# Kernel optimization log

Hardware: AMD Instinct MI355X
Metric: run time of the kernel (lower is better)

The kernel has to match this reference:

```python
import jax, jax.numpy as jnp
import numpy as np

B, T, D, H = 1024, 128, 300, 100
FORGET_BIAS = 1.0


def _lstm_final_c(x, W, b):
    """Run a BasicLSTMCell over x:[B,T,D]; return final cell state c:[B,H].
    Gate order (TF BasicLSTMCell): i, j, f, o from [x,h] @ W + b, W:[D+H,4H].
    """
    Bv = x.shape[0]
    c0 = jnp.zeros((Bv, H), x.dtype)
    h0 = jnp.zeros((Bv, H), x.dtype)

    def step(carry, xt):
        c, h = carry
        z = jnp.concatenate([xt, h], axis=-1) @ W + b  # [B,4H]
        i, j, f, o = jnp.split(z, 4, axis=-1)
        c2 = c * jax.nn.sigmoid(f + FORGET_BIAS) + jax.nn.sigmoid(i) * jnp.tanh(j)
        h2 = jnp.tanh(c2) * jax.nn.sigmoid(o)
        return (c2, h2), None

    (cT, _), _ = jax.lax.scan(step, (c0, h0), jnp.swapaxes(x, 0, 1))  # scan over time
    return cT


def _bi_rnn_c(x, W_fw, b_fw, W_bw, b_bw):
    # full sequence_length => backward cell consumes time-reversed input
    c_fw = _lstm_final_c(x, W_fw, b_fw)
    c_bw = _lstm_final_c(x[:, ::-1, :], W_bw, b_bw)
    return jnp.concatenate([c_fw, c_bw], axis=1)  # [B,2H]


def setup_inputs() -> dict:
    key = jax.random.key(0)
    ks = jax.random.split(key, 6)
    s = 0.05
    return {
        "premises": jax.random.normal(ks[0], (B, T, D), jnp.float32),
        "hypotheses": jax.random.normal(ks[1], (B, T, D), jnp.float32),
        "Wp_fw": jax.random.normal(ks[2], (D + H, 4 * H), jnp.float32) * s,
        "bp_fw": jnp.zeros((4 * H,), jnp.float32),
        "Wp_bw": jax.random.normal(ks[3], (D + H, 4 * H), jnp.float32) * s,
        "bp_bw": jnp.zeros((4 * H,), jnp.float32),
        "Wh_fw": jax.random.normal(ks[4], (D + H, 4 * H), jnp.float32) * s,
        "bh_fw": jnp.zeros((4 * H,), jnp.float32),
        "Wh_bw": jax.random.normal(ks[5], (D + H, 4 * H), jnp.float32) * s,
        "bh_bw": jnp.zeros((4 * H,), jnp.float32),
    }


def reference(premises, hypotheses, Wp_fw, bp_fw, Wp_bw, bp_bw,
              Wh_fw, bh_fw, Wh_bw, bh_bw):
    premise_out = _bi_rnn_c(premises, Wp_fw, bp_fw, Wp_bw, bp_bw)      # [B,2H]
    hypothesis_out = _bi_rnn_c(hypotheses, Wh_fw, bh_fw, Wh_bw, bh_bw)  # [B,2H]
    return jnp.concatenate([premise_out, hypothesis_out], axis=1)      # [B,4H]
```

## Files before the change

kernel.cpp:

```cpp
#include <hip/hip_runtime.h>
#include <hip/hip_bf16.h>

#define T_STEPS 128
#define D_IN    300
#define H_DIM   100
#define KDIM    400
#define KSTRIDE 424
#define WAVES   8
#define BLOCK   (WAVES * 64)
#define MROWS   16
#define NRES    3
#define LN2E    1.44269504f
#define LN2E2   2.88539008f

typedef __attribute__((ext_vector_type(8))) short bf16x8;
typedef __attribute__((ext_vector_type(4))) float f32x4;

__device__ __forceinline__ ushort f2bf(float f) {
    uint u = __float_as_uint(f);
    u += 0x7FFFu + ((u >> 16) & 1u);
    return (ushort)(u >> 16);
}
__device__ __forceinline__ uint cvt_pk_bf16(float lo, float hi) {
    uint r;
    asm("v_cvt_pk_bf16_f32 %0, %1, %2" : "=v"(r) : "v"(lo), "v"(hi));
    return r;
}
__device__ __forceinline__ bf16x8 gload16(const ushort* p) {
    bf16x8 r;
    asm volatile("global_load_dwordx4 %0, %1, off" : "=v"(r) : "v"(p));
    return r;
}

__device__ __forceinline__ float lstm_gate(const f32x4 z, float& c) {
    float ei = __builtin_amdgcn_exp2f(-z[0]);
    float ej = __builtin_amdgcn_exp2f(fminf(-z[1], 126.0f));
    float ef = __builtin_amdgcn_exp2f(-z[2]);
    float eo = __builtin_amdgcn_exp2f(-z[3]);
    float rf  = __builtin_amdgcn_rcpf(1.0f + ef);
    float rij = __builtin_amdgcn_rcpf((1.0f + ei) * (1.0f + ej));
    float c2 = c * rf + (1.0f - ej) * rij;
    c = c2;
    float ec = __builtin_amdgcn_exp2f(fminf(-LN2E2 * c2, 126.0f));
    return (1.0f - ec) * __builtin_amdgcn_rcpf((1.0f + ec) * (1.0f + eo));
}

__global__ __launch_bounds__(256) void prep_w(
    const float* __restrict__ W0, const float* __restrict__ W1,
    const float* __restrict__ W2, const float* __restrict__ W3,
    ushort* __restrict__ Wt)
{
    int idx = blockIdx.x * 256 + threadIdx.x;
    const int total = 4 * 400 * KSTRIDE;
    if (idx >= total) return;
    int c   = idx / (400 * KSTRIDE);
    int rem = idx - c * (400 * KSTRIDE);
    int p   = rem / KSTRIDE;
    int k   = rem - p * KSTRIDE;
    const float* W = (c == 0) ? W0 : (c == 1) ? W1 : (c == 2) ? W2 : W3;
    const int g = p & 3;
    const float scale = (g == 1) ? LN2E2 : LN2E;
    float v = 0.0f;
    if (k < KDIM) v = W[k * 400 + g * 100 + (p >> 2)] * scale;
    Wt[idx] = f2bf(v);
}

__global__ __launch_bounds__(BLOCK, 2) void lstm_mfma(
    const float* __restrict__ premises,
    const float* __restrict__ hypotheses,
    const float* __restrict__ b0, const float* __restrict__ b1,
    const float* __restrict__ b2, const float* __restrict__ b3,
    const ushort* __restrict__ Wt,
    float* __restrict__ out)
{
    __shared__ ushort xh[2][MROWS * KSTRIDE];
    __shared__ ushort b24[13 * 512];

    const int tid = threadIdx.x;
    const int l   = tid & 63;
    const int w   = tid >> 6;
    const int combo = blockIdx.y;
    const int row0  = blockIdx.x * MROWS;
    const bool backward = (combo & 1) != 0;
    const float* x    = (combo < 2) ? premises : hypotheses;
    const float* bias = (combo == 0) ? b0 : (combo == 1) ? b1 : (combo == 2) ? b2 : b3;
    const ushort* Wc  = Wt + (size_t)combo * 400 * KSTRIDE;

    const int bn = l & 15;
    const int ul = l >> 4;

    bf16x8 bfr[NRES][13];
    #pragma unroll
    for (int i = 0; i < NRES; ++i) {
        const ushort* bp = Wc + (size_t)((3 * w + i) * 16 + bn) * KSTRIDE + ul * 8;
        #pragma unroll
        for (int ks = 0; ks < 13; ++ks)
            bfr[i][ks] = gload16(bp + ks * 32);
    }
    asm volatile("s_waitcnt vmcnt(0)" ::: "memory");

    const bool hasS = (w == WAVES - 1);
    if (w == 0) {
        const ushort* bp = Wc + (size_t)(24 * 16 + bn) * KSTRIDE + ul * 8;
        #pragma unroll
        for (int ks = 0; ks < 13; ++ks)
            *reinterpret_cast<bf16x8*>(&b24[ks * 512 + l * 8]) =
                *reinterpret_cast<const bf16x8*>(bp + ks * 32);
    }

    float bv[NRES][4], bvS[4] = {0.f, 0.f, 0.f, 0.f};
    #pragma unroll
    for (int i = 0; i < NRES; ++i) {
        int u = (3 * w + i) * 4 + ul;
        bv[i][0] = LN2E * bias[u];
        bv[i][1] = LN2E2 * bias[100 + u];
        bv[i][2] = LN2E * (bias[200 + u] + 1.0f);
        bv[i][3] = LN2E * bias[300 + u];
    }
    if (hasS) {
        int u = 96 + ul;
        bvS[0] = LN2E * bias[u];
        bvS[1] = LN2E2 * bias[100 + u];
        bvS[2] = LN2E * (bias[200 + u] + 1.0f);
        bvS[3] = LN2E * bias[300 + u];
    }

    for (int i = tid; i < 2 * MROWS * (KSTRIDE - KDIM); i += BLOCK) {
        int b = i / (MROWS * (KSTRIDE - KDIM));
        int j = i - b * (MROWS * (KSTRIDE - KDIM));
        int r = j / (KSTRIDE - KDIM);
        int k = KDIM + (j - r * (KSTRIDE - KDIM));
        xh[b][r * KSTRIDE + k] = 0;
    }
    for (int i = tid; i < MROWS * H_DIM; i += BLOCK) {
        int r = i / H_DIM;
        xh[0][r * KSTRIDE + D_IN + (i - r * H_DIM)] = 0;
    }
    {
        int t0 = backward ? (T_STEPS - 1) : 0;
        for (int c = tid; c < 1200; c += BLOCK) {
            int r = c / 75, cc = c - (c / 75) * 75;
            float4 v = *reinterpret_cast<const float4*>(
                x + ((size_t)(row0 + r) * T_STEPS + t0) * D_IN + cc * 4);
            uint2 q;
            q.x = cvt_pk_bf16(v.x, v.y);
            q.y = cvt_pk_bf16(v.z, v.w);
            *reinterpret_cast<uint2*>(&xh[0][r * KSTRIDE + cc * 4]) = q;
        }
    }
    __syncthreads();

    const uint a_off = (uint)(l & 15) * KSTRIDE + (uint)(l >> 4) * 8;
    const int  row   = l & 15;
    const bool stager = (tid < 448);
    const int sc0 = tid, sc1 = tid + 448, sc2 = tid + 896;
    const int sr0 = sc0 / 75, sd0 = sc0 - sr0 * 75;
    const int sr1 = sc1 / 75, sd1 = sc1 - sr1 * 75;
    const int sr2 = sc2 / 75, sd2 = sc2 - sr2 * 75;
    const bool has2 = (sc2 < 1200);

    float creg0 = 0.f, creg1 = 0.f, creg2 = 0.f, cregS = 0.f;

    float4 A0, A1, A2, B0, B1, B2;

    if (stager) {
        int tn = backward ? (T_STEPS - 2) : 1;
        A0 = *reinterpret_cast<const float4*>(
            x + ((size_t)(row0 + sr0) * T_STEPS + tn) * D_IN + sd0 * 4);
        A1 = *reinterpret_cast<const float4*>(
            x + ((size_t)(row0 + sr1) * T_STEPS + tn) * D_IN + sd1 * 4);
        if (has2)
            A2 = *reinterpret_cast<const float4*>(
                x + ((size_t)(row0 + sr2) * T_STEPS + tn) * D_IN + sd2 * 4);
    }

    auto step = [&](int t, float4& i0, float4& i1, float4& i2,
                           float4& u0, float4& u1, float4& u2) {
        const ushort* cur = &xh[t & 1][0];
        ushort* nxt = &xh[(t & 1) ^ 1][0];

        if (t < T_STEPS - 2 && stager) {
            int tn = backward ? (T_STEPS - 3 - t) : (t + 2);
            i0 = *reinterpret_cast<const float4*>(
                x + ((size_t)(row0 + sr0) * T_STEPS + tn) * D_IN + sd0 * 4);
            i1 = *reinterpret_cast<const float4*>(
                x + ((size_t)(row0 + sr1) * T_STEPS + tn) * D_IN + sd1 * 4);
            if (has2)
                i2 = *reinterpret_cast<const float4*>(
                    x + ((size_t)(row0 + sr2) * T_STEPS + tn) * D_IN + sd2 * 4);
        }

        f32x4 acc0 = {bv[0][0], bv[0][1], bv[0][2], bv[0][3]};
        f32x4 acc1 = {bv[1][0], bv[1][1], bv[1][2], bv[1][3]};
        f32x4 acc2 = {bv[2][0], bv[2][1], bv[2][2], bv[2][3]};
        f32x4 accS = {bvS[0], bvS[1], bvS[2], bvS[3]};
        #pragma unroll
        for (int ks = 0; ks < 13; ++ks) {
            const bf16x8 a = *reinterpret_cast<const bf16x8*>(cur + a_off + ks * 32);
            acc0 = __builtin_amdgcn_mfma_f32_16x16x32_bf16(bfr[0][ks], a, acc0, 0, 0, 0);
            acc1 = __builtin_amdgcn_mfma_f32_16x16x32_bf16(bfr[1][ks], a, acc1, 0, 0, 0);
            acc2 = __builtin_amdgcn_mfma_f32_16x16x32_bf16(bfr[2][ks], a, acc2, 0, 0, 0);
            if (hasS) {
                const bf16x8 bs = *reinterpret_cast<const bf16x8*>(&b24[ks * 512 + l * 8]);
                accS = __builtin_amdgcn_mfma_f32_16x16x32_bf16(bs, a, accS, 0, 0, 0);
            }
        }

        float h0 = lstm_gate(acc0, creg0);
        float h1 = lstm_gate(acc1, creg1);
        float h2 = lstm_gate(acc2, creg2);
        uint pk01 = cvt_pk_bf16(h0, h1);
        uint pk2  = cvt_pk_bf16(h2, h2);
        ushort* hdst = nxt + row * KSTRIDE + D_IN + (3 * w) * 4 + ul;
        hdst[0] = (ushort)(pk01 & 0xFFFFu);
        hdst[4] = (ushort)(pk01 >> 16);
        hdst[8] = (ushort)(pk2 & 0xFFFFu);
        if (hasS) {
            float hS = lstm_gate(accS, cregS);
            nxt[row * KSTRIDE + D_IN + 96 + ul] = (ushort)(cvt_pk_bf16(hS, hS) & 0xFFFFu);
        }

        if (t < T_STEPS - 1 && stager) {
            uint2 q;
            q.x = cvt_pk_bf16(u0.x, u0.y);
            q.y = cvt_pk_bf16(u0.z, u0.w);
            *reinterpret_cast<uint2*>(&nxt[sr0 * KSTRIDE + sd0 * 4]) = q;
            q.x = cvt_pk_bf16(u1.x, u1.y);
            q.y = cvt_pk_bf16(u1.z, u1.w);
            *reinterpret_cast<uint2*>(&nxt[sr1 * KSTRIDE + sd1 * 4]) = q;
            if (has2) {
                q.x = cvt_pk_bf16(u2.x, u2.y);
                q.y = cvt_pk_bf16(u2.z, u2.w);
                *reinterpret_cast<uint2*>(&nxt[sr2 * KSTRIDE + sd2 * 4]) = q;
            }
        }
        __syncthreads();
    };

    for (int t = 0; t < T_STEPS; t += 2) {
        step(t,     B0, B1, B2, A0, A1, A2);
        step(t + 1, A0, A1, A2, B0, B1, B2);
    }

    out[(size_t)(row0 + row) * 400 + combo * 100 + (3 * w) * 4 + ul]     = creg0;
    out[(size_t)(row0 + row) * 400 + combo * 100 + (3 * w + 1) * 4 + ul] = creg1;
    out[(size_t)(row0 + row) * 400 + combo * 100 + (3 * w + 2) * 4 + ul] = creg2;
    if (hasS)
        out[(size_t)(row0 + row) * 400 + combo * 100 + 96 + ul] = cregS;
}

extern "C" void kernel_launch(void* const* d_in, const int* in_sizes, int n_in,
                              void* d_out, int out_size, void* d_ws, size_t ws_size,
                              hipStream_t stream) {
    const float* premises   = (const float*)d_in[0];
    const float* hypotheses = (const float*)d_in[1];
    const float* Wp_fw = (const float*)d_in[2];
    const float* bp_fw = (const float*)d_in[3];
    const float* Wp_bw = (const float*)d_in[4];
    const float* bp_bw = (const float*)d_in[5];
    const float* Wh_fw = (const float*)d_in[6];
    const float* bh_fw = (const float*)d_in[7];
    const float* Wh_bw = (const float*)d_in[8];
    const float* bh_bw = (const float*)d_in[9];
    float* out = (float*)d_out;
    ushort* Wt = (ushort*)d_ws;

    {
        const int total = 4 * 400 * KSTRIDE;
        prep_w<<<(total + 255) / 256, 256, 0, stream>>>(Wp_fw, Wp_bw, Wh_fw, Wh_bw, Wt);
    }
    dim3 grid(1024 / MROWS, 4);
    lstm_mfma<<<grid, dim3(BLOCK), 0, stream>>>(
        premises, hypotheses,
        bp_fw, bp_bw, bh_fw, bh_bw,
        Wt, out);
}
```

Baseline: 223.6 us.

## Split LSTM GEMM into x-projection and recurrent parts, precompute next step's input term

Splits the per-step K=400 MFMA into an input part (first 288 x features) and a recurrent part (h plus the remaining 12 x features). The input part for step t+1 is computed after the gates of step t, off the serial h dependency chain. A triple-buffered x tile and a double-buffered h tile in shared memory support this. The block shrinks from 8 to 4 waves, each owning 6 gate tiles, which raises register pressure and halves occupancy.

```diff
diff --git a/kernel.cpp b/kernel.cpp
--- a/kernel.cpp
+++ b/kernel.cpp
@@ -5,11 +5,15 @@
 #define D_IN    300
 #define H_DIM   100
 #define KDIM    400
-#define KSTRIDE 424
-#define WAVES   8
-#define BLOCK   (WAVES * 64)
+#define WK      416
+#define XK      288
 #define MROWS   16
-#define NRES    3
+#define XROW    296
+#define XSLOT   (MROWS * XROW)
+#define HROW    136
+#define HSLOT   (MROWS * HROW)
+#define BLOCK   256
+#define NRES    6
 #define LN2E    1.44269504f
 #define LN2E2   2.88539008f
 
@@ -24,11 +28,6 @@
 __device__ __forceinline__ uint cvt_pk_bf16(float lo, float hi) {
     uint r;
     asm("v_cvt_pk_bf16_f32 %0, %1, %2" : "=v"(r) : "v"(lo), "v"(hi));
-    return r;
-}
-__device__ __forceinline__ bf16x8 gload16(const ushort* p) {
-    bf16x8 r;
-    asm volatile("global_load_dwordx4 %0, %1, off" : "=v"(r) : "v"(p));
     return r;
 }
 
@@ -51,12 +50,12 @@
     ushort* __restrict__ Wt)
 {
     int idx = blockIdx.x * 256 + threadIdx.x;
-    const int total = 4 * 400 * KSTRIDE;
+    const int total = 4 * 400 * WK;
     if (idx >= total) return;
-    int c   = idx / (400 * KSTRIDE);
-    int rem = idx - c * (400 * KSTRIDE);
-    int p   = rem / KSTRIDE;
-    int k   = rem - p * KSTRIDE;
+    int c   = idx / (400 * WK);
+    int rem = idx - c * (400 * WK);
+    int p   = rem / WK;
+    int k   = rem - p * WK;
     const float* W = (c == 0) ? W0 : (c == 1) ? W1 : (c == 2) ? W2 : W3;
     const int g = p & 3;
     const float scale = (g == 1) ? LN2E2 : LN2E;
@@ -65,7 +64,7 @@
     Wt[idx] = f2bf(v);
 }
 
-__global__ __launch_bounds__(BLOCK, 2) void lstm_mfma(
+__global__ __launch_bounds__(BLOCK, 1) void lstm_mfma(
     const float* __restrict__ premises,
     const float* __restrict__ hypotheses,
     const float* __restrict__ b0, const float* __restrict__ b1,
@@ -73,7 +72,8 @@
     const ushort* __restrict__ Wt,
     float* __restrict__ out)
 {
-    __shared__ ushort xh[2][MROWS * KSTRIDE];
+    __shared__ ushort xmain[3 * XSLOT];
+    __shared__ ushort hbuf[2 * HSLOT];
     __shared__ ushort b24[13 * 512];
 
     const int tid = threadIdx.x;
@@ -84,7 +84,7 @@
     const bool backward = (combo & 1) != 0;
     const float* x    = (combo < 2) ? premises : hypotheses;
     const float* bias = (combo == 0) ? b0 : (combo == 1) ? b1 : (combo == 2) ? b2 : b3;
-    const ushort* Wc  = Wt + (size_t)combo * 400 * KSTRIDE;
+    const ushort* Wc  = Wt + (size_t)combo * 400 * WK;
 
     const int bn = l & 15;
     const int ul = l >> 4;
@@ -92,16 +92,14 @@
     bf16x8 bfr[NRES][13];
     #pragma unroll
     for (int i = 0; i < NRES; ++i) {
-        const ushort* bp = Wc + (size_t)((3 * w + i) * 16 + bn) * KSTRIDE + ul * 8;
+        const ushort* bp = Wc + (size_t)((NRES * w + i) * 16 + bn) * WK + ul * 8;
         #pragma unroll
         for (int ks = 0; ks < 13; ++ks)
-            bfr[i][ks] = gload16(bp + ks * 32);
-    }
-    asm volatile("s_waitcnt vmcnt(0)" ::: "memory");
-
-    const bool hasS = (w == WAVES - 1);
+            bfr[i][ks] = *reinterpret_cast<const bf16x8*>(bp + ks * 32);
+    }
+    const bool hasS = (w == 3);
     if (w == 0) {
-        const ushort* bp = Wc + (size_t)(24 * 16 + bn) * KSTRIDE + ul * 8;
+        const ushort* bp = Wc + (size_t)(24 * 16 + bn) * WK + ul * 8;
         #pragma unroll
         for (int ks = 0; ks < 13; ++ks)
             *reinterpret_cast<bf16x8*>(&b24[ks * 512 + l * 8]) =
@@ -111,7 +109,7 @@
     float bv[NRES][4], bvS[4] = {0.f, 0.f, 0.f, 0.f};
     #pragma unroll
     for (int i = 0; i < NRES; ++i) {
-        int u = (3 * w + i) * 4 + ul;
+        int u = (NRES * w + i) * 4 + ul;
         bv[i][0] = LN2E * bias[u];
         bv[i][1] = LN2E2 * bias[100 + u];
         bv[i][2] = LN2E * (bias[200 + u] + 1.0f);
@@ -125,126 +123,169 @@
         bvS[3] = LN2E * bias[300 + u];
     }
 
-    for (int i = tid; i < 2 * MROWS * (KSTRIDE - KDIM); i += BLOCK) {
-        int b = i / (MROWS * (KSTRIDE - KDIM));
-        int j = i - b * (MROWS * (KSTRIDE - KDIM));
-        int r = j / (KSTRIDE - KDIM);
-        int k = KDIM + (j - r * (KSTRIDE - KDIM));
-        xh[b][r * KSTRIDE + k] = 0;
-    }
-    for (int i = tid; i < MROWS * H_DIM; i += BLOCK) {
-        int r = i / H_DIM;
-        xh[0][r * KSTRIDE + D_IN + (i - r * H_DIM)] = 0;
-    }
-    {
-        int t0 = backward ? (T_STEPS - 1) : 0;
-        for (int c = tid; c < 1200; c += BLOCK) {
-            int r = c / 75, cc = c - (c / 75) * 75;
+    int MR[5], MD[5];
+    bool MV[5];
+    #pragma unroll
+    for (int j = 0; j < 5; ++j) {
+        int c = tid + j * 256;
+        MV[j] = (c < 1152);
+        MR[j] = c / 72;
+        MD[j] = c - MR[j] * 72;
+    }
+    const bool tv = (tid < 48);
+    const int TR = tid / 3, TD = tid - TR * 3;
+
+    float4 T1, T2;
+
+    for (int s = 0; s < 2; ++s) {
+        int tt = backward ? (T_STEPS - 1 - s) : s;
+        #pragma unroll
+        for (int j = 0; j < 5; ++j)
+            if (MV[j]) {
+                float4 v = *reinterpret_cast<const float4*>(
+                    x + ((size_t)(row0 + MR[j]) * T_STEPS + tt) * D_IN + MD[j] * 4);
+                uint2 q;
+                q.x = cvt_pk_bf16(v.x, v.y);
+                q.y = cvt_pk_bf16(v.z, v.w);
+                *reinterpret_cast<uint2*>(&xmain[s * XSLOT + MR[j] * XROW + MD[j] * 4]) = q;
+            }
+        if (tv) {
             float4 v = *reinterpret_cast<const float4*>(
-                x + ((size_t)(row0 + r) * T_STEPS + t0) * D_IN + cc * 4);
+                x + ((size_t)(row0 + TR) * T_STEPS + tt) * D_IN + XK + TD * 4);
+            if (s == 0) {
+                uint2 q;
+                q.x = cvt_pk_bf16(v.x, v.y);
+                q.y = cvt_pk_bf16(v.z, v.w);
+                *reinterpret_cast<uint2*>(&hbuf[TR * HROW + TD * 4]) = q;
+            } else {
+                T1 = v;
+            }
+        }
+    }
+    for (int i = tid; i < MROWS * 124; i += BLOCK) {
+        int r = i / 124;
+        hbuf[r * HROW + 12 + (i - r * 124)] = 0;
+    }
+    for (int i = tid; i < MROWS * 24; i += BLOCK) {
+        int r = i / 24;
+        hbuf[HSLOT + r * HROW + 112 + (i - r * 24)] = 0;
+    }
+    __syncthreads();
+
+    const uint xoff = (uint)(l & 15) * XROW + (uint)ul * 8;
+    const uint hoff = (uint)(l & 15) * HROW + (uint)ul * 8;
+    const int  row  = l & 15;
+
+    f32x4 accA[NRES], accB[NRES], accAS, accBS;
+    #pragma unroll
+    for (int i = 0; i < NRES; ++i)
+        accA[i] = (f32x4){bv[i][0], bv[i][1], bv[i][2], bv[i][3]};
+    accAS = (f32x4){bvS[0], bvS[1], bvS[2], bvS[3]};
+    #pragma unroll
+    for (int ks = 0; ks < 9; ++ks) {
+        const bf16x8 a = *reinterpret_cast<const bf16x8*>(xmain + xoff + ks * 32);
+        #pragma unroll
+        for (int i = 0; i < NRES; ++i)
+            accA[i] = __builtin_amdgcn_mfma_f32_16x16x32_bf16(bfr[i][ks], a, accA[i], 0, 0, 0);
+        if (hasS) {
+            const bf16x8 bs = *reinterpret_cast<const bf16x8*>(&b24[ks * 512 + l * 8]);
+            accAS = __builtin_amdgcn_mfma_f32_16x16x32_bf16(bs, a, accAS, 0, 0, 0);
+        }
+    }
+
+    float creg[NRES];
+    #pragma unroll
+    for (int i = 0; i < NRES; ++i) creg[i] = 0.f;
+    float cregS = 0.f;
+
+    auto body = [&](int t, f32x4 (&accC)[NRES], f32x4& accCS,
+                           f32x4 (&accN)[NRES], f32x4& accNS,
+                           float4& Tw, float4& Ti) {
+        float4 M[5];
+        if (t <= T_STEPS - 3) {
+            int tn = backward ? (T_STEPS - 3 - t) : (t + 2);
+            #pragma unroll
+            for (int j = 0; j < 5; ++j)
+                if (MV[j])
+                    M[j] = *reinterpret_cast<const float4*>(
+                        x + ((size_t)(row0 + MR[j]) * T_STEPS + tn) * D_IN + MD[j] * 4);
+            if (tv)
+                Ti = *reinterpret_cast<const float4*>(
+                    x + ((size_t)(row0 + TR) * T_STEPS + tn) * D_IN + XK + TD * 4);
+        }
+
+        const ushort* hb = hbuf + (t & 1) * HSLOT;
+        #pragma unroll
+        for (int ks = 0; ks < 4; ++ks) {
+            const bf16x8 a = *reinterpret_cast<const bf16x8*>(hb + hoff + ks * 32);
+            #pragma unroll
+            for (int i = 0; i < NRES; ++i)
+                accC[i] = __builtin_amdgcn_mfma_f32_16x16x32_bf16(bfr[i][9 + ks], a, accC[i], 0, 0, 0);
+            if (hasS) {
+                const bf16x8 bs = *reinterpret_cast<const bf16x8*>(&b24[(9 + ks) * 512 + l * 8]);
+                accCS = __builtin_amdgcn_mfma_f32_16x16x32_bf16(bs, a, accCS, 0, 0, 0);
+            }
+        }
+
+        ushort* hw = hbuf + ((t + 1) & 1) * HSLOT;
+        #pragma unroll
+        for (int i = 0; i < NRES; ++i) {
+            float h = lstm_gate(accC[i], creg[i]);
+            hw[row * HROW + 12 + (NRES * w + i) * 4 + ul] =
+                (ushort)(cvt_pk_bf16(h, h) & 0xFFFFu);
+        }
+        if (hasS) {
+            float hS = lstm_gate(accCS, cregS);
+            hw[row * HROW + 12 + 96 + ul] = (ushort)(cvt_pk_bf16(hS, hS) & 0xFFFFu);
+        }
+        if (tv && t <= T_STEPS - 2) {
             uint2 q;
-            q.x = cvt_pk_bf16(v.x, v.y);
-            q.y = cvt_pk_bf16(v.z, v.w);
-            *reinterpret_cast<uint2*>(&xh[0][r * KSTRIDE + cc * 4]) = q;
-        }
-    }
-    __syncthreads();
-
-    const uint a_off = (uint)(l & 15) * KSTRIDE + (uint)(l >> 4) * 8;
-    const int  row   = l & 15;
-    const bool stager = (tid < 448);
-    const int sc0 = tid, sc1 = tid + 448, sc2 = tid + 896;
-    const int sr0 = sc0 / 75, sd0 = sc0 - sr0 * 75;
-    const int sr1 = sc1 / 75, sd1 = sc1 - sr1 * 75;
-    const int sr2 = sc2 / 75, sd2 = sc2 - sr2 * 75;
-    const bool has2 = (sc2 < 1200);
-
-    float creg0 = 0.f, creg1 = 0.f, creg2 = 0.f, cregS = 0.f;
-
-    float4 A0, A1, A2, B0, B1, B2;
-
-    if (stager) {
-        int tn = backward ? (T_STEPS - 2) : 1;
-        A0 = *reinterpret_cast<const float4*>(
-            x + ((size_t)(row0 + sr0) * T_STEPS + tn) * D_IN + sd0 * 4);
-        A1 = *reinterpret_cast<const float4*>(
-            x + ((size_t)(row0 + sr1) * T_STEPS + tn) * D_IN + sd1 * 4);
-        if (has2)
-            A2 = *reinterpret_cast<const float4*>(
-                x + ((size_t)(row0 + sr2) * T_STEPS + tn) * D_IN + sd2 * 4);
-    }
-
-    auto step = [&](int t, float4& i0, float4& i1, float4& i2,
-                           float4& u0, float4& u1, float4& u2) {
-        const ushort* cur = &xh[t & 1][0];
-        ushort* nxt = &xh[(t & 1) ^ 1][0];
-
-        if (t < T_STEPS - 2 && stager) {
-            int tn = backward ? (T_STEPS - 3 - t) : (t + 2);
-            i0 = *reinterpret_cast<const float4*>(
-                x + ((size_t)(row0 + sr0) * T_STEPS + tn) * D_IN + sd0 * 4);
-            i1 = *reinterpret_cast<const float4*>(
-                x + ((size_t)(row0 + sr1) * T_STEPS + tn) * D_IN + sd1 * 4);
-            if (has2)
-                i2 = *reinterpret_cast<const float4*>(
-                    x + ((size_t)(row0 + sr2) * T_STEPS + tn) * D_IN + sd2 * 4);
-        }
-
-        f32x4 acc0 = {bv[0][0], bv[0][1], bv[0][2], bv[0][3]};
-        f32x4 acc1 = {bv[1][0], bv[1][1], bv[1][2], bv[1][3]};
-        f32x4 acc2 = {bv[2][0], bv[2][1], bv[2][2], bv[2][3]};
-        f32x4 accS = {bvS[0], bvS[1], bvS[2], bvS[3]};
-        #pragma unroll
-        for (int ks = 0; ks < 13; ++ks) {
-            const bf16x8 a = *reinterpret_cast<const bf16x8*>(cur + a_off + ks * 32);
-            acc0 = __builtin_amdgcn_mfma_f32_16x16x32_bf16(bfr[0][ks], a, acc0, 0, 0, 0);
-            acc1 = __builtin_amdgcn_mfma_f32_16x16x32_bf16(bfr[1][ks], a, acc1, 0, 0, 0);
-            acc2 = __builtin_amdgcn_mfma_f32_16x16x32_bf16(bfr[2][ks], a, acc2, 0, 0, 0);
-            if (hasS) {
-                const bf16x8 bs = *reinterpret_cast<const bf16x8*>(&b24[ks * 512 + l * 8]);
-                accS = __builtin_amdgcn_mfma_f32_16x16x32_bf16(bs, a, accS, 0, 0, 0);
+            q.x = cvt_pk_bf16(Tw.x, Tw.y);
+            q.y = cvt_pk_bf16(Tw.z, Tw.w);
+            *reinterpret_cast<uint2*>(&hw[TR * HROW + TD * 4]) = q;
+        }
+
+        if (t <= T_STEPS - 2) {
+            const ushort* xr = xmain + ((t + 1) % 3) * XSLOT;
+            #pragma unroll
+            for (int i = 0; i < NRES; ++i)
+                accN[i] = (f32x4){bv[i][0], bv[i][1], bv[i][2], bv[i][3]};
+            accNS = (f32x4){bvS[0], bvS[1], bvS[2], bvS[3]};
+            #pragma unroll
+            for (int ks = 0; ks < 9; ++ks) {
+                const bf16x8 a = *reinterpret_cast<const bf16x8*>(xr + xoff + ks * 32);
+                #pragma unroll
+                for (int i = 0; i < NRES; ++i)
+                    accN[i] = __builtin_amdgcn_mfma_f32_16x16x32_bf16(bfr[i][ks], a, accN[i], 0, 0, 0);
+                if (hasS) {
+                    const bf16x8 bs = *reinterpret_cast<const bf16x8*>(&b24[ks * 512 + l * 8]);
+                    accNS = __builtin_amdgcn_mfma_f32_16x16x32_bf16(bs, a, accNS, 0, 0, 0);
+                }
             }
         }
 
-        float h0 = lstm_gate(acc0, creg0);
-        float h1 = lstm_gate(acc1, creg1);
-        float h2 = lstm_gate(acc2, creg2);
-        uint pk01 = cvt_pk_bf16(h0, h1);
-        uint pk2  = cvt_pk_bf16(h2, h2);
-        ushort* hdst = nxt + row * KSTRIDE + D_IN + (3 * w) * 4 + ul;
-        hdst[0] = (ushort)(pk01 & 0xFFFFu);
-        hdst[4] = (ushort)(pk01 >> 16);
-        hdst[8] = (ushort)(pk2 & 0xFFFFu);
-        if (hasS) {
-            float hS = lstm_gate(accS, cregS);
-            nxt[row * KSTRIDE + D_IN + 96 + ul] = (ushort)(cvt_pk_bf16(hS, hS) & 0xFFFFu);
-        }
-
-        if (t < T_STEPS - 1 && stager) {
-            uint2 q;
-            q.x = cvt_pk_bf16(u0.x, u0.y);
-            q.y = cvt_pk_bf16(u0.z, u0.w);
-            *reinterpret_cast<uint2*>(&nxt[sr0 * KSTRIDE + sd0 * 4]) = q;
-            q.x = cvt_pk_bf16(u1.x, u1.y);
-            q.y = cvt_pk_bf16(u1.z, u1.w);
-            *reinterpret_cast<uint2*>(&nxt[sr1 * KSTRIDE + sd1 * 4]) = q;
-            if (has2) {
-                q.x = cvt_pk_bf16(u2.x, u2.y);
-                q.y = cvt_pk_bf16(u2.z, u2.w);
-                *reinterpret_cast<uint2*>(&nxt[sr2 * KSTRIDE + sd2 * 4]) = q;
-            }
+        if (t <= T_STEPS - 3) {
+            ushort* xw = xmain + ((t + 2) % 3) * XSLOT;
+            #pragma unroll
+            for (int j = 0; j < 5; ++j)
+                if (MV[j]) {
+                    uint2 q;
+                    q.x = cvt_pk_bf16(M[j].x, M[j].y);
+                    q.y = cvt_pk_bf16(M[j].z, M[j].w);
+                    *reinterpret_cast<uint2*>(&xw[MR[j] * XROW + MD[j] * 4]) = q;
+                }
         }
         __syncthreads();
     };
 
     for (int t = 0; t < T_STEPS; t += 2) {
-        step(t,     B0, B1, B2, A0, A1, A2);
-        step(t + 1, A0, A1, A2, B0, B1, B2);
-    }
-
-    out[(size_t)(row0 + row) * 400 + combo * 100 + (3 * w) * 4 + ul]     = creg0;
-    out[(size_t)(row0 + row) * 400 + combo * 100 + (3 * w + 1) * 4 + ul] = creg1;
-    out[(size_t)(row0 + row) * 400 + combo * 100 + (3 * w + 2) * 4 + ul] = creg2;
+        body(t,     accA, accAS, accB, accBS, T1, T2);
+        body(t + 1, accB, accBS, accA, accAS, T2, T1);
+    }
+
+    #pragma unroll
+    for (int i = 0; i < NRES; ++i)
+        out[(size_t)(row0 + row) * 400 + combo * 100 + (NRES * w + i) * 4 + ul] = creg[i];
     if (hasS)
         out[(size_t)(row0 + row) * 400 + combo * 100 + 96 + ul] = cregS;
 }
@@ -266,7 +307,7 @@
     ushort* Wt = (ushort*)d_ws;
 
     {
-        const int total = 4 * 400 * KSTRIDE;
+        const int total = 4 * 400 * WK;
         prep_w<<<(total + 255) / 256, 256, 0, stream>>>(Wp_fw, Wp_bw, Wh_fw, Wh_bw, Wt);
     }
     dim3 grid(1024 / MROWS, 4);
```

New measurement: 320.4 us. +43.3%, slower.
